# Kernel optimization log

Hardware: AMD Instinct MI355X
Metric: run time of the kernel (lower is better)

## Reference

```python
import jax, jax.numpy as jnp
import numpy as np

N_NODES = 100000
N_EDGES = 1600000
N_FEAT, N_HID, N_CLS = 256, 64, 16


def setup_inputs() -> dict:
    key = jax.random.key(0)
    ks = jax.random.split(key, 8)
    x = jax.random.normal(ks[0], (N_NODES, N_FEAT), dtype=jnp.float32)
    adj_row = jax.random.randint(ks[1], (N_EDGES,), 0, N_NODES, dtype=jnp.int32)
    adj_col = jax.random.randint(ks[2], (N_EDGES,), 0, N_NODES, dtype=jnp.int32)
    adj_vals = jax.random.uniform(ks[3], (N_EDGES,), dtype=jnp.float32)
    W1 = jax.random.normal(ks[4], (N_FEAT, N_HID), dtype=jnp.float32) * 0.05
    b1 = jnp.zeros((N_HID,), dtype=jnp.float32)
    W2 = jax.random.normal(ks[5], (N_HID, N_CLS), dtype=jnp.float32) * 0.05
    b2 = jnp.zeros((N_CLS,), dtype=jnp.float32)
    return {"x": x, "adj_row": adj_row, "adj_col": adj_col, "adj_vals": adj_vals,
            "W1": W1, "b1": b1, "W2": W2, "b2": b2}


def _spmm(row, col, vals, h):
    # sparse [N,N] @ dense [N,D]: gather source rows, scale, scatter-add to dest rows
    msgs = vals[:, None] * h[col]                       # [E, D]
    return jax.ops.segment_sum(msgs, row, num_segments=N_NODES)


def reference(x, adj_row, adj_col, adj_vals, W1, b1, W2, b2):
    # layer 1: linear -> spmm -> relu  (dropout is identity at inference)
    h = _spmm(adj_row, adj_col, adj_vals, x @ W1 + b1)  # [N, n_hidden]
    h = jax.nn.relu(h)
    # layer 2: linear -> spmm -> log_softmax
    out = _spmm(adj_row, adj_col, adj_vals, h @ W2 + b2)  # [N, n_class]
    return jax.nn.log_softmax(out, axis=1)
```

## Files before the change

kernel.cpp:

```cpp
#include <hip/hip_runtime.h>

#define N_NODES 100000
#define N_EDGES 1600000
#define N_FEAT  256
#define N_HID   64
#define N_CLS   16
#define NB      391
#define CHUNK   8192
#define NSCAT   196
#define NGEMM1  1563
#define NHIST   256

typedef unsigned short bfraw;
typedef unsigned int uint32;

typedef __attribute__((ext_vector_type(8))) short  bf16x8;
typedef __attribute__((ext_vector_type(4))) float  f32x4;

__device__ __forceinline__ bfraw f2bf(float f) {
    union { float f; unsigned int i; } v; v.f = f;
    unsigned int x = v.i;
    return (bfraw)((x + 0x7FFFu + ((x >> 16) & 1u)) >> 16);
}

__device__ __forceinline__ float bf_lo(uint32 g) { return __uint_as_float(g << 16); }
__device__ __forceinline__ float bf_hi(uint32 g) { return __uint_as_float(g & 0xFFFF0000u); }

__global__ __launch_bounds__(256) void w1cvt_hist_k(const float* __restrict__ W1,
                                                    bfraw* __restrict__ w1f,
                                                    const int* __restrict__ rowi,
                                                    int* __restrict__ part) {
    __shared__ int lh[NB];
    if (blockIdx.x < 64) {
        int i = blockIdx.x * 256 + threadIdx.x;
        int k = i >> 6, n = i & 63;
        w1f[((size_t)((k >> 3) * 64 + n) << 3) + (k & 7)] = f2bf(W1[i]);
        return;
    }
    const int hb = blockIdx.x - 64;
    for (int i = threadIdx.x; i < NB; i += 256) lh[i] = 0;
    __syncthreads();
    const int4* r4p = (const int4*)rowi;
    for (int i = hb * 256 + threadIdx.x; i < N_EDGES / 4; i += 256 * 256) {
        int4 r = r4p[i];
        atomicAdd(&lh[r.x >> 8], 1);
        atomicAdd(&lh[r.y >> 8], 1);
        atomicAdd(&lh[r.z >> 8], 1);
        atomicAdd(&lh[r.w >> 8], 1);
    }
    __syncthreads();
    for (int i = threadIdx.x; i < NB; i += 256)
        part[hb * NB + i] = lh[i];
}

__global__ __launch_bounds__(512) void bscan_k(const int* __restrict__ part,
                                               int* __restrict__ bbase,
                                               int* __restrict__ gcur,
                                               int* __restrict__ rp) {
    __shared__ int s[512];
    int t = threadIdx.x;
    int v = 0;
    if (t < NB) {
        #pragma unroll 8
        for (int hb = 0; hb < NHIST; ++hb) v += part[hb * NB + t];
    }
    s[t] = v;
    __syncthreads();
    #pragma unroll
    for (int off = 1; off < 512; off <<= 1) {
        int x = (t >= off) ? s[t - off] : 0;
        __syncthreads();
        s[t] += x;
        __syncthreads();
    }
    if (t <= NB) {
        int b = s[t] - v;
        bbase[t] = b;
        if (t < NB) gcur[t] = b;
    }
    if (t == 0) rp[N_NODES] = N_EDGES;
}

__global__ __launch_bounds__(1024) void scatter_k(const int* __restrict__ rowi,
                                                  const int* __restrict__ coli,
                                                  const float* __restrict__ vals,
                                                  int* __restrict__ gcur,
                                                  int2* __restrict__ edges) {
    __shared__ int lh[NB];
    __shared__ int lb[NB];
    const int t    = threadIdx.x;
    const int e0   = blockIdx.x * CHUNK;
    const bool full = (e0 + CHUNK <= N_EDGES);
    for (int i = t; i < NB; i += 1024) lh[i] = 0;
    __syncthreads();

    int4 r4[2];
    if (full) {
        const int4* rp4 = (const int4*)(rowi + e0);
        #pragma unroll
        for (int u = 0; u < 2; ++u) r4[u] = rp4[t + u * 1024];
        #pragma unroll
        for (int u = 0; u < 2; ++u) {
            atomicAdd(&lh[r4[u].x >> 8], 1);
            atomicAdd(&lh[r4[u].y >> 8], 1);
            atomicAdd(&lh[r4[u].z >> 8], 1);
            atomicAdd(&lh[r4[u].w >> 8], 1);
        }
    } else {
        for (int j = t; j < CHUNK; j += 1024) {
            int e = e0 + j;
            if (e < N_EDGES) atomicAdd(&lh[rowi[e] >> 8], 1);
        }
    }
    __syncthreads();
    for (int i = t; i < NB; i += 1024) {
        int c = lh[i];
        lb[i] = c ? atomicAdd(&gcur[i], c) : 0;
        lh[i] = 0;
    }
    __syncthreads();
    if (full) {
        const int4*   cp4 = (const int4*)(coli + e0);
        const float4* vp4 = (const float4*)(vals + e0);
        #pragma unroll
        for (int u = 0; u < 2; ++u) {
            int4   c4 = cp4[t + u * 1024];
            float4 v4 = vp4[t + u * 1024];
            int r, b, rk;
            r = r4[u].x; b = r >> 8; rk = atomicAdd(&lh[b], 1);
            edges[lb[b] + rk] = make_int2(c4.x | ((r & 255) << 17), __float_as_int(v4.x));
            r = r4[u].y; b = r >> 8; rk = atomicAdd(&lh[b], 1);
            edges[lb[b] + rk] = make_int2(c4.y | ((r & 255) << 17), __float_as_int(v4.y));
            r = r4[u].z; b = r >> 8; rk = atomicAdd(&lh[b], 1);
            edges[lb[b] + rk] = make_int2(c4.z | ((r & 255) << 17), __float_as_int(v4.z));
            r = r4[u].w; b = r >> 8; rk = atomicAdd(&lh[b], 1);
            edges[lb[b] + rk] = make_int2(c4.w | ((r & 255) << 17), __float_as_int(v4.w));
        }
    } else {
        for (int j = t; j < CHUNK; j += 1024) {
            int e = e0 + j;
            if (e < N_EDGES) {
                int r  = rowi[e];
                int b  = r >> 8;
                int rk = atomicAdd(&lh[b], 1);
                edges[lb[b] + rk] = make_int2(coli[e] | ((r & 255) << 17),
                                              __float_as_int(vals[e]));
            }
        }
    }
}

__global__ __launch_bounds__(256) void sort_gemm1_k(const int* __restrict__ bbase,
                                                    const int2* __restrict__ edges,
                                                    int2* __restrict__ edges2,
                                                    int* __restrict__ rp,
                                                    const float* __restrict__ x,
                                                    const bfraw* __restrict__ w1f,
                                                    const float* __restrict__ b1,
                                                    bfraw* __restrict__ h0) {
    __shared__ int cnt[256];
    __shared__ int pos[256];
    const int t = threadIdx.x;

    if (blockIdx.x < NB) {
        const int b   = blockIdx.x;
        const int beg = bbase[b];
        const int end = bbase[b + 1];

        cnt[t] = 0;
        __syncthreads();
        {
            int i = beg + t;
            for (; i + 768 < end; i += 1024) {
                int2 a = edges[i], c = edges[i + 256], d = edges[i + 512], e = edges[i + 768];
                atomicAdd(&cnt[(a.x >> 17) & 255], 1);
                atomicAdd(&cnt[(c.x >> 17) & 255], 1);
                atomicAdd(&cnt[(d.x >> 17) & 255], 1);
                atomicAdd(&cnt[(e.x >> 17) & 255], 1);
            }
            for (; i < end; i += 256)
                atomicAdd(&cnt[(edges[i].x >> 17) & 255], 1);
        }
        __syncthreads();

        int v = cnt[t];
        pos[t] = v;
        __syncthreads();
        #pragma unroll
        for (int off = 1; off < 256; off <<= 1) {
            int y = (t >= off) ? pos[t - off] : 0;
            __syncthreads();
            pos[t] += y;
            __syncthreads();
        }
        int excl = pos[t] - v;

        int row = (b << 8) + t;
        if (row < N_NODES) rp[row] = beg + excl;
        __syncthreads();
        pos[t] = excl;
        __syncthreads();

        {
            int i = beg + t;
            for (; i + 768 < end; i += 1024) {
                int2 E0 = edges[i], E1 = edges[i + 256], E2 = edges[i + 512], E3 = edges[i + 768];
                int r0 = (E0.x >> 17) & 255, r1 = (E1.x >> 17) & 255;
                int r2 = (E2.x >> 17) & 255, r3 = (E3.x >> 17) & 255;
                int k0 = atomicAdd(&pos[r0], 1);
                int k1 = atomicAdd(&pos[r1], 1);
                int k2 = atomicAdd(&pos[r2], 1);
                int k3 = atomicAdd(&pos[r3], 1);
                edges2[beg + k0] = make_int2(E0.x & 0x1FFFF, E0.y);
                edges2[beg + k1] = make_int2(E1.x & 0x1FFFF, E1.y);
                edges2[beg + k2] = make_int2(E2.x & 0x1FFFF, E2.y);
                edges2[beg + k3] = make_int2(E3.x & 0x1FFFF, E3.y);
            }
            for (; i < end; i += 256) {
                int2 E = edges[i];
                int r  = (E.x >> 17) & 255;
                int rk = atomicAdd(&pos[r], 1);
                edges2[beg + rk] = make_int2(E.x & 0x1FFFF, E.y);
            }
        }
        return;
    }

    const int bg   = blockIdx.x - NB;
    const int w    = t >> 6;
    const int lane = t & 63;
    const int q    = lane >> 4;
    const int m    = lane & 15;

    const int row  = bg * 64 + w * 16 + m;
    const int srow = row < N_NODES ? row : N_NODES - 1;
    const float* xp = x + (size_t)srow * N_FEAT + q * 8;
    const bf16x8* w1v = (const bf16x8*)w1f;

    f32x4 acc[4];
    #pragma unroll
    for (int nt = 0; nt < 4; ++nt) acc[nt] = (f32x4){0.f, 0.f, 0.f, 0.f};

    #pragma unroll
    for (int s = 0; s < 8; ++s) {
        float4 a0 = *(const float4*)(xp + s * 32);
        float4 a1 = *(const float4*)(xp + s * 32 + 4);
        bf16x8 af;
        af[0] = (short)f2bf(a0.x); af[1] = (short)f2bf(a0.y);
        af[2] = (short)f2bf(a0.z); af[3] = (short)f2bf(a0.w);
        af[4] = (short)f2bf(a1.x); af[5] = (short)f2bf(a1.y);
        af[6] = (short)f2bf(a1.z); af[7] = (short)f2bf(a1.w);
        const int g = s * 4 + q;
        #pragma unroll
        for (int nt = 0; nt < 4; ++nt) {
            bf16x8 bf_ = w1v[g * 64 + nt * 16 + m];
            acc[nt] = __builtin_amdgcn_mfma_f32_16x16x32_bf16(af, bf_, acc[nt], 0, 0, 0);
        }
    }

    float bb[4];
    #pragma unroll
    for (int nt = 0; nt < 4; ++nt) bb[nt] = b1[nt * 16 + m];

    const int orow0 = bg * 64 + w * 16 + q * 4;
    #pragma unroll
    for (int r = 0; r < 4; ++r) {
        int orow = orow0 + r;
        if (orow < N_NODES) {
            bfraw* op = h0 + (size_t)orow * N_HID + m;
            #pragma unroll
            for (int nt = 0; nt < 4; ++nt)
                op[nt * 16] = f2bf(acc[nt][r] + bb[nt]);
        }
    }
}

__global__ __launch_bounds__(256) void spmm1_fused3_k(const int* __restrict__ rp,
                                                      const int2* __restrict__ edges2,
                                                      const uint32* __restrict__ h0p,
                                                      const float* __restrict__ W2,
                                                      const float* __restrict__ b2,
                                                      float* __restrict__ h2) {
    __shared__ float Hs[16][68];
    __shared__ float Ws[64 * 16];
    __shared__ float bs[16];
    const int t = threadIdx.x;
    *(float4*)&Ws[t * 4] = ((const float4*)W2)[t];
    if (t < 16) bs[t] = b2[t];

    const int g16 = t >> 4;
    const int l   = t & 15;
    const int row = blockIdx.x * 16 + g16;
    const int beg = rp[row];
    const int end = rp[row + 1];

    const uint2* h0v = (const uint2*)h0p;

    float a0 = 0.f, a1 = 0.f, a2 = 0.f, a3 = 0.f;
    int i = beg;
    for (; i + 8 <= end; i += 8) {
        int2 E[8];
        #pragma unroll
        for (int u = 0; u < 8; ++u) E[u] = edges2[i + u];
        uint2 q[8];
        #pragma unroll
        for (int u = 0; u < 8; ++u) q[u] = h0v[(size_t)E[u].x * 16 + l];
        #pragma unroll
        for (int u = 0; u < 8; ++u) {
            float v = __int_as_float(E[u].y);
            a0 += v * bf_lo(q[u].x); a1 += v * bf_hi(q[u].x);
            a2 += v * bf_lo(q[u].y); a3 += v * bf_hi(q[u].y);
        }
    }
    for (; i + 4 <= end; i += 4) {
        int2 E[4];
        #pragma unroll
        for (int u = 0; u < 4; ++u) E[u] = edges2[i + u];
        uint2 q[4];
        #pragma unroll
        for (int u = 0; u < 4; ++u) q[u] = h0v[(size_t)E[u].x * 16 + l];
        #pragma unroll
        for (int u = 0; u < 4; ++u) {
            float v = __int_as_float(E[u].y);
            a0 += v * bf_lo(q[u].x); a1 += v * bf_hi(q[u].x);
            a2 += v * bf_lo(q[u].y); a3 += v * bf_hi(q[u].y);
        }
    }
    for (; i < end; ++i) {
        int2 E = edges2[i];
        uint2 q = h0v[(size_t)E.x * 16 + l];
        float v = __int_as_float(E.y);
        a0 += v * bf_lo(q.x); a1 += v * bf_hi(q.x);
        a2 += v * bf_lo(q.y); a3 += v * bf_hi(q.y);
    }

    *(float4*)&Hs[g16][4 * l] = make_float4(fmaxf(a0, 0.f), fmaxf(a1, 0.f),
                                            fmaxf(a2, 0.f), fmaxf(a3, 0.f));
    __syncthreads();

    const int r = t >> 4;
    const int c = t & 15;
    float a = bs[c];
    #pragma unroll
    for (int k = 0; k < 64; ++k)
        a += Hs[r][k] * Ws[k * 16 + c];
    h2[(size_t)(blockIdx.x * 16 + r) * N_CLS + c] = a;
}

__global__ __launch_bounds__(256) void spmm2_lsm_k(const int* __restrict__ rp,
                                                   const int2* __restrict__ edges2,
                                                   const float* __restrict__ h2,
                                                   float* __restrict__ outp) {
    const int l   = threadIdx.x & 7;
    const int row = blockIdx.x * 32 + (threadIdx.x >> 3);
    const int beg = rp[row];
    const int end = rp[row + 1];
    const float2* h2v = (const float2*)h2;

    float a0 = 0.f, a1 = 0.f;
    int i = beg;
    for (; i + 8 <= end; i += 8) {
        int2 e[8];
        #pragma unroll
        for (int u = 0; u < 8; ++u) e[u] = edges2[i + u];
        float2 g[8];
        #pragma unroll
        for (int u = 0; u < 8; ++u) g[u] = h2v[(size_t)e[u].x * 8 + l];
        #pragma unroll
        for (int u = 0; u < 8; ++u) {
            float v = __int_as_float(e[u].y);
            a0 += v * g[u].x; a1 += v * g[u].y;
        }
    }
    for (; i + 4 <= end; i += 4) {
        int2 e[4];
        #pragma unroll
        for (int u = 0; u < 4; ++u) e[u] = edges2[i + u];
        float2 g[4];
        #pragma unroll
        for (int u = 0; u < 4; ++u) g[u] = h2v[(size_t)e[u].x * 8 + l];
        #pragma unroll
        for (int u = 0; u < 4; ++u) {
            float v = __int_as_float(e[u].y);
            a0 += v * g[u].x; a1 += v * g[u].y;
        }
    }
    for (; i < end; ++i) {
        int2 e = edges2[i];
        float2 g = h2v[(size_t)e.x * 8 + l];
        float v = __int_as_float(e.y);
        a0 += v * g.x; a1 += v * g.y;
    }

    float m = fmaxf(a0, a1);
    #pragma unroll
    for (int off = 4; off; off >>= 1) m = fmaxf(m, __shfl_xor(m, off, 8));
    float ex = expf(a0 - m) + expf(a1 - m);
    float s = ex;
    #pragma unroll
    for (int off = 4; off; off >>= 1) s += __shfl_xor(s, off, 8);
    float ls = logf(s);
    *(float2*)(outp + (size_t)row * N_CLS + 2 * l) =
        make_float2(a0 - m - ls, a1 - m - ls);
}

extern "C" void kernel_launch(void* const* d_in, const int* in_sizes, int n_in,
                              void* d_out, int out_size, void* d_ws, size_t ws_size,
                              hipStream_t stream) {
    const float* x        = (const float*)d_in[0];
    const int*   adj_row  = (const int*)d_in[1];
    const int*   adj_col  = (const int*)d_in[2];
    const float* adj_vals = (const float*)d_in[3];
    const float* W1       = (const float*)d_in[4];
    const float* b1       = (const float*)d_in[5];
    const float* W2       = (const float*)d_in[6];
    const float* b2       = (const float*)d_in[7];
    float*       out      = (float*)d_out;

    const size_t H0_BYTES = (size_t)N_NODES * N_HID * sizeof(bfraw);
    const size_t H2_BYTES = (size_t)N_NODES * N_CLS * sizeof(float);
    const size_t E_BYTES  = (size_t)N_EDGES * sizeof(int2);
    bfraw* h0     = (bfraw*)d_ws;
    float* h2     = (float*)((char*)d_ws + H0_BYTES);
    int2*  edges  = (int2*)((char*)h2 + H2_BYTES);
    int2*  edges2 = (int2*)((char*)edges + E_BYTES);
    int*   bbase  = (int*)((char*)edges2 + E_BYTES);
    int*   gcur   = bbase + NB + 1;
    int*   rp     = gcur + NB;
    bfraw* w1f    = (bfraw*)(rp + N_NODES + 1);
    int*   part   = (int*)(w1f + 16384);

    w1cvt_hist_k<<<320, 256, 0, stream>>>(W1, w1f, adj_row, part);
    bscan_k<<<1, 512, 0, stream>>>(part, bbase, gcur, rp);
    scatter_k<<<NSCAT, 1024, 0, stream>>>(adj_row, adj_col, adj_vals, gcur, edges);
    sort_gemm1_k<<<NB + NGEMM1, 256, 0, stream>>>(bbase, edges, edges2, rp,
                                                  x, w1f, b1, h0);

    spmm1_fused3_k<<<N_NODES / 16, 256, 0, stream>>>(rp, edges2, (const uint32*)h0,
                                                     W2, b2, h2);

    spmm2_lsm_k<<<N_NODES / 32, 256, 0, stream>>>(rp, edges2, h2, out);
}
```

Before: 281.6 us.

## Remove single-block scan kernel by recomputing bucket bases inside consumers

Drops the separate single-block scan launch. Each scatter block now recomputes the exclusive prefix of bucket counts redundantly, and each sort block reduces its own begin and end offsets directly from the partial histograms. The histogram grid is cut from 256 to 64 blocks so these redundant reductions stay cheap, and gcur is zeroed in the first kernel. The trade is one fewer launch and serial tiny kernel against redundant scan work in 196 scatter blocks and a larger per-block reduction in the sort blocks.

Measured after the change: 298.9 us. +6.2%, slower.

```diff
diff --git a/kernel.cpp b/kernel.cpp
--- a/kernel.cpp
+++ b/kernel.cpp
@@ -9,7 +9,7 @@
 #define CHUNK   8192
 #define NSCAT   196
 #define NGEMM1  1563
-#define NHIST   256
+#define NHIST   64
 
 typedef unsigned short bfraw;
 typedef unsigned int uint32;
@@ -29,19 +29,22 @@
 __global__ __launch_bounds__(256) void w1cvt_hist_k(const float* __restrict__ W1,
                                                     bfraw* __restrict__ w1f,
                                                     const int* __restrict__ rowi,
-                                                    int* __restrict__ part) {
+                                                    int* __restrict__ part,
+                                                    int* __restrict__ gcur) {
     __shared__ int lh[NB];
     if (blockIdx.x < 64) {
         int i = blockIdx.x * 256 + threadIdx.x;
         int k = i >> 6, n = i & 63;
         w1f[((size_t)((k >> 3) * 64 + n) << 3) + (k & 7)] = f2bf(W1[i]);
+        if (blockIdx.x == 0)
+            for (int j = threadIdx.x; j < NB; j += 256) gcur[j] = 0;
         return;
     }
     const int hb = blockIdx.x - 64;
     for (int i = threadIdx.x; i < NB; i += 256) lh[i] = 0;
     __syncthreads();
     const int4* r4p = (const int4*)rowi;
-    for (int i = hb * 256 + threadIdx.x; i < N_EDGES / 4; i += 256 * 256) {
+    for (int i = hb * 256 + threadIdx.x; i < N_EDGES / 4; i += NHIST * 256) {
         int4 r = r4p[i];
         atomicAdd(&lh[r.x >> 8], 1);
         atomicAdd(&lh[r.y >> 8], 1);
@@ -53,45 +56,36 @@
         part[hb * NB + i] = lh[i];
 }
 
-__global__ __launch_bounds__(512) void bscan_k(const int* __restrict__ part,
-                                               int* __restrict__ bbase,
-                                               int* __restrict__ gcur,
-                                               int* __restrict__ rp) {
-    __shared__ int s[512];
-    int t = threadIdx.x;
-    int v = 0;
-    if (t < NB) {
-        #pragma unroll 8
-        for (int hb = 0; hb < NHIST; ++hb) v += part[hb * NB + t];
-    }
-    s[t] = v;
-    __syncthreads();
-    #pragma unroll
-    for (int off = 1; off < 512; off <<= 1) {
-        int x = (t >= off) ? s[t - off] : 0;
-        __syncthreads();
-        s[t] += x;
-        __syncthreads();
-    }
-    if (t <= NB) {
-        int b = s[t] - v;
-        bbase[t] = b;
-        if (t < NB) gcur[t] = b;
-    }
-    if (t == 0) rp[N_NODES] = N_EDGES;
-}
-
 __global__ __launch_bounds__(1024) void scatter_k(const int* __restrict__ rowi,
                                                   const int* __restrict__ coli,
                                                   const float* __restrict__ vals,
+                                                  const int* __restrict__ part,
                                                   int* __restrict__ gcur,
                                                   int2* __restrict__ edges) {
     __shared__ int lh[NB];
     __shared__ int lb[NB];
+    __shared__ int gb[NB];
+    __shared__ int s[512];
     const int t    = threadIdx.x;
     const int e0   = blockIdx.x * CHUNK;
     const bool full = (e0 + CHUNK <= N_EDGES);
+
+    int myCnt = 0;
+    if (t < NB) {
+        #pragma unroll 8
+        for (int hb = 0; hb < NHIST; ++hb) myCnt += part[hb * NB + t];
+    }
+    if (t < 512) s[t] = myCnt;
     for (int i = t; i < NB; i += 1024) lh[i] = 0;
+    __syncthreads();
+    #pragma unroll
+    for (int off = 1; off < 512; off <<= 1) {
+        int x = (t < 512 && t >= off) ? s[t - off] : 0;
+        __syncthreads();
+        if (t < 512) s[t] += x;
+        __syncthreads();
+    }
+    if (t < NB) gb[t] = s[t] - myCnt;
     __syncthreads();
 
     int4 r4[2];
@@ -115,7 +109,7 @@
     __syncthreads();
     for (int i = t; i < NB; i += 1024) {
         int c = lh[i];
-        lb[i] = c ? atomicAdd(&gcur[i], c) : 0;
+        lb[i] = c ? (gb[i] + atomicAdd(&gcur[i], c)) : 0;
         lh[i] = 0;
     }
     __syncthreads();
@@ -150,7 +144,7 @@
     }
 }
 
-__global__ __launch_bounds__(256) void sort_gemm1_k(const int* __restrict__ bbase,
+__global__ __launch_bounds__(256) void sort_gemm1_k(const int* __restrict__ part,
                                                     const int2* __restrict__ edges,
                                                     int2* __restrict__ edges2,
                                                     int* __restrict__ rp,
@@ -160,12 +154,35 @@
                                                     bfraw* __restrict__ h0) {
     __shared__ int cnt[256];
     __shared__ int pos[256];
+    __shared__ int red[256];
     const int t = threadIdx.x;
 
     if (blockIdx.x < NB) {
-        const int b   = blockIdx.x;
-        const int beg = bbase[b];
-        const int end = bbase[b + 1];
+        const int b = blockIdx.x;
+
+        int acc = 0;
+        for (int hb = 0; hb < NHIST; ++hb)
+            for (int i = t; i < b; i += 256) acc += part[hb * NB + i];
+        red[t] = acc;
+        __syncthreads();
+        #pragma unroll
+        for (int off = 128; off; off >>= 1) {
+            if (t < off) red[t] += red[t + off];
+            __syncthreads();
+        }
+        const int beg = red[0];
+        __syncthreads();
+        int own = (t < NHIST) ? part[t * NB + b] : 0;
+        red[t] = own;
+        __syncthreads();
+        #pragma unroll
+        for (int off = 128; off; off >>= 1) {
+            if (t < off) red[t] += red[t + off];
+            __syncthreads();
+        }
+        const int end = beg + red[0];
+        __syncthreads();
+        if (b == 0 && t == 0) rp[N_NODES] = N_EDGES;
 
         cnt[t] = 0;
         __syncthreads();
@@ -424,16 +441,15 @@
     float* h2     = (float*)((char*)d_ws + H0_BYTES);
     int2*  edges  = (int2*)((char*)h2 + H2_BYTES);
     int2*  edges2 = (int2*)((char*)edges + E_BYTES);
-    int*   bbase  = (int*)((char*)edges2 + E_BYTES);
-    int*   gcur   = bbase + NB + 1;
+    int*   gcur   = (int*)((char*)edges2 + E_BYTES);
     int*   rp     = gcur + NB;
     bfraw* w1f    = (bfraw*)(rp + N_NODES + 1);
     int*   part   = (int*)(w1f + 16384);
 
-    w1cvt_hist_k<<<320, 256, 0, stream>>>(W1, w1f, adj_row, part);
-    bscan_k<<<1, 512, 0, stream>>>(part, bbase, gcur, rp);
-    scatter_k<<<NSCAT, 1024, 0, stream>>>(adj_row, adj_col, adj_vals, gcur, edges);
-    sort_gemm1_k<<<NB + NGEMM1, 256, 0, stream>>>(bbase, edges, edges2, rp,
+    w1cvt_hist_k<<<128, 256, 0, stream>>>(W1, w1f, adj_row, part, gcur);
+    scatter_k<<<NSCAT, 1024, 0, stream>>>(adj_row, adj_col, adj_vals, part,
+                                          gcur, edges);
+    sort_gemm1_k<<<NB + NGEMM1, 256, 0, stream>>>(part, edges, edges2, rp,
                                                   x, w1f, b1, h0);
 
     spmm1_fused3_k<<<N_NODES / 16, 256, 0, stream>>>(rp, edges2, (const uint32*)h0,
```
